# Performance work log

Hardware: AMD Instinct MI355X
Metric: run time of the kernel (lower is better)

Reference implementation:

```python
import jax, jax.numpy as jnp
import numpy as np

B, S, E, H = 4, 2048, 512, 8
DK = E // H  # 64 quantum wires per head


def setup_inputs() -> dict:
    key = jax.random.key(0)
    k1, k2, k3, k4 = jax.random.split(key, 4)
    x = jax.random.normal(k1, (B, S, E), dtype=jnp.float32)
    theta = jax.random.normal(k2, (DK,), dtype=jnp.float32)
    W = jax.random.normal(k3, (E, E), dtype=jnp.float32) * (1.0 / np.sqrt(E))
    b = jax.random.normal(k4, (E,), dtype=jnp.float32) * 0.01
    return {"x": x, "theta": theta, "W": W, "b": b}


def _quantum_project(x, theta):
    # x: [B,S,E] -> heads [B,H,S,DK]. Circuit per wire: RX(x_i) then RX(theta_i),
    # product state => <Z_i> = cos(x_i + theta_i).
    xh = x.reshape(B, S, H, DK).transpose(0, 2, 1, 3)  # [B,H,S,DK]
    return jnp.cos(xh + theta)


def reference(x, theta, W, b):
    q = _quantum_project(x, theta)
    k = _quantum_project(x, theta)
    v = _quantum_project(x, theta)
    scores = jnp.einsum('bhqd,bhkd->bhqk', q, k) / jnp.sqrt(jnp.float32(DK))
    attn = jax.nn.softmax(scores, axis=-1)  # dropout is identity in eval
    out = jnp.einsum('bhqk,bhkd->bhqd', attn, v)  # [B,H,S,DK]
    out = out.transpose(0, 2, 1, 3).reshape(B, S, E)
    return out @ W.T + b
```

## Files before the change

kernel.cpp:

```cpp
#include <hip/hip_runtime.h>
#include <hip/hip_bf16.h>
#include <math.h>

#define B_ 4
#define S_ 2048
#define E_ 512
#define H_ 8
#define DK_ 64

typedef __attribute__((ext_vector_type(8))) short short8;
typedef __attribute__((ext_vector_type(4))) float f32x4;
typedef _Float16 half8 __attribute__((ext_vector_type(8)));
typedef _Float16 half4 __attribute__((ext_vector_type(4)));

__device__ inline short8 ld8(const void* p) {
  return *reinterpret_cast<const short8*>(p);
}

static __device__ inline short8 cvt8h(float4 a, float4 b) {
  half8 r;
  r[0] = (_Float16)a.x; r[1] = (_Float16)a.y; r[2] = (_Float16)a.z; r[3] = (_Float16)a.w;
  r[4] = (_Float16)b.x; r[5] = (_Float16)b.y; r[6] = (_Float16)b.z; r[7] = (_Float16)b.w;
  return __builtin_bit_cast(short8, r);
}

__global__ __launch_bounds__(256) void prep_g_kernel(
    const float* __restrict__ x, const float* __restrict__ theta,
    _Float16* __restrict__ g, _Float16* __restrict__ gTh) {
  int bh = blockIdx.y;
  int b = bh >> 3, h = bh & 7;
  int s0 = blockIdx.x * 64;
  __shared__ _Float16 tile[64][68];
  int tid = threadIdx.x;
  const float* xp = x + ((size_t)(b * S_ + s0)) * E_ + h * DK_;
  _Float16* gp = g + ((size_t)bh * S_ + s0) * DK_;
#pragma unroll
  for (int it = 0; it < 16; ++it) {
    int idx = it * 256 + tid;
    int sr = idx >> 6, dc = idx & 63;
    float val = __cosf(xp[(size_t)sr * E_ + dc] + theta[dc]);
    gp[sr * DK_ + dc] = (_Float16)val;
    tile[sr][dc] = (_Float16)val;
  }
  __syncthreads();
  _Float16* gTp = gTh + ((size_t)bh * DK_) * S_ + s0;
#pragma unroll
  for (int it = 0; it < 16; ++it) {
    int idx = it * 256 + tid;
    int dr = idx >> 6, sc = idx & 63;
    gTp[(size_t)dr * S_ + sc] = tile[sc][dr];
  }
}

__global__ __launch_bounds__(256, 3) void attn_kernel(
    const _Float16* __restrict__ g, const _Float16* __restrict__ gTh,
    _Float16* __restrict__ ao) {
  const int tid = threadIdx.x;
  const int wave = tid >> 6, lane = tid & 63;
  const int col = lane & 15, quad = lane >> 4;
  const int bh = blockIdx.y;
  const int q0 = blockIdx.x * 64;
  const _Float16* gp = g + (size_t)bh * S_ * DK_;
  const _Float16* gvp = gTh + (size_t)bh * DK_ * S_;

  __shared__ short smem[2 * 64 * 72];
  short* kt = smem;
  short* vt = smem + 64 * 72;

  const int srow = tid >> 3;
  const int soct = (tid & 7) * 8;
  const int sd0 = srow * 72 + soct;
  const int sd1 = (srow + 32) * 72 + soct;
  const _Float16* kg0 = gp + tid * 8;
  const _Float16* kg1 = gp + (tid + 256) * 8;
  const _Float16* vg0 = gvp + (size_t)srow * S_ + (tid & 7) * 8;
  const _Float16* vg1 = gvp + (size_t)(srow + 32) * S_ + (tid & 7) * 8;

  short8 kr0 = ld8(kg0), kr1 = ld8(kg1), vr0 = ld8(vg0), vr1 = ld8(vg1);

  *reinterpret_cast<short8*>(kt + sd0) = ld8(gp + (size_t)q0 * DK_ + tid * 8);
  *reinterpret_cast<short8*>(kt + sd1) = ld8(gp + (size_t)q0 * DK_ + (tid + 256) * 8);
  __syncthreads();
  const _Float16 hC1 = (_Float16)0.18033688011112042f;
  half8 qa[4][2];
#pragma unroll
  for (int qc = 0; qc < 4; ++qc) {
    const short* qp = kt + (qc * 16 + col) * 72 + quad * 8;
    qa[qc][0] = *reinterpret_cast<const half8*>(qp) * hC1;
    qa[qc][1] = *reinterpret_cast<const half8*>(qp + 32) * hC1;
  }
  __syncthreads();

  f32x4 o[4][4];
#pragma unroll
  for (int qc = 0; qc < 4; ++qc)
#pragma unroll
    for (int dc = 0; dc < 4; ++dc) o[qc][dc] = f32x4{0.f, 0.f, 0.f, 0.f};
  float l[4] = {0.f, 0.f, 0.f, 0.f};

  for (int kk = 0; kk < S_; kk += 64) {
    *reinterpret_cast<short8*>(kt + sd0) = kr0;
    *reinterpret_cast<short8*>(kt + sd1) = kr1;
    *reinterpret_cast<short8*>(vt + sd0) = vr0;
    *reinterpret_cast<short8*>(vt + sd1) = vr1;
    __syncthreads();

    if (kk + 64 < S_) {
      kr0 = ld8(kg0 + (kk + 64) * 64);
      kr1 = ld8(kg1 + (kk + 64) * 64);
      vr0 = ld8(vg0 + kk + 64);
      vr1 = ld8(vg1 + kk + 64);
    }

    const short* kp = kt + (wave * 16 + col) * 72 + quad * 8;
    half8 kf0 = *reinterpret_cast<const half8*>(kp);
    half8 kf1 = *reinterpret_cast<const half8*>(kp + 32);

    half4 pf[4];
#pragma unroll
    for (int qc = 0; qc < 4; ++qc) {
      f32x4 z{0.f, 0.f, 0.f, 0.f};
      z = __builtin_amdgcn_mfma_f32_16x16x32_f16(kf0, qa[qc][0], z, 0, 0, 0);
      z = __builtin_amdgcn_mfma_f32_16x16x32_f16(kf1, qa[qc][1], z, 0, 0, 0);
      float p0 = __builtin_amdgcn_exp2f(z[0]);
      float p1 = __builtin_amdgcn_exp2f(z[1]);
      float p2 = __builtin_amdgcn_exp2f(z[2]);
      float p3 = __builtin_amdgcn_exp2f(z[3]);
      l[qc] += (p0 + p1) + (p2 + p3);
      half4 pk;
      pk[0] = (_Float16)p0; pk[1] = (_Float16)p1;
      pk[2] = (_Float16)p2; pk[3] = (_Float16)p3;
      pf[qc] = pk;
    }

#pragma unroll
    for (int dc = 0; dc < 4; ++dc) {
      half4 vf = *reinterpret_cast<const half4*>(
          vt + (dc * 16 + col) * 72 + wave * 16 + quad * 4);
#pragma unroll
      for (int qc = 0; qc < 4; ++qc)
        o[qc][dc] = __builtin_amdgcn_mfma_f32_16x16x16f16(vf, pf[qc], o[qc][dc], 0, 0, 0);
    }
    __syncthreads();
  }

#pragma unroll
  for (int qc = 0; qc < 4; ++qc) {
    float t = l[qc];
    t += __shfl_xor(t, 16);
    t += __shfl_xor(t, 32);
    l[qc] = t;
  }
  float* red = (float*)smem;
  if (quad == 0) {
#pragma unroll
    for (int qc = 0; qc < 4; ++qc) red[(wave * 4 + qc) * 16 + col] = l[qc];
  }
  __syncthreads();
  float ltot = 0.f;
#pragma unroll
  for (int w2 = 0; w2 < 4; ++w2) ltot += red[(w2 * 4 + wave) * 16 + col];
  float inv = __builtin_amdgcn_rcpf(ltot);

  int b = bh >> 3, h = bh & 7;
  float* ored = (float*)smem;
#pragma unroll
  for (int qc = 0; qc < 4; ++qc) {
    __syncthreads();
#pragma unroll
    for (int dc = 0; dc < 4; ++dc)
      *reinterpret_cast<f32x4*>(ored + wave * 1024 + lane * 16 + dc * 4) = o[qc][dc];
    __syncthreads();
    if (wave == qc) {
      _Float16* op = ao + ((size_t)b * S_ + (q0 + qc * 16 + col)) * E_ + h * DK_;
#pragma unroll
      for (int dc = 0; dc < 4; ++dc) {
        f32x4 acc = *reinterpret_cast<const f32x4*>(ored + lane * 16 + dc * 4);
#pragma unroll
        for (int w2 = 1; w2 < 4; ++w2)
          acc = acc + *reinterpret_cast<const f32x4*>(ored + w2 * 1024 + lane * 16 + dc * 4);
        half4 pk;
        pk[0] = (_Float16)(acc[0] * inv);
        pk[1] = (_Float16)(acc[1] * inv);
        pk[2] = (_Float16)(acc[2] * inv);
        pk[3] = (_Float16)(acc[3] * inv);
        *reinterpret_cast<half4*>(op + dc * 16 + quad * 4) = pk;
      }
    }
  }
}

__global__ __launch_bounds__(256) void proj_kernel(
    const _Float16* __restrict__ ao, const float* __restrict__ W,
    const float* __restrict__ bias, float* __restrict__ out) {
  const int tid = threadIdx.x;
  const int wave = tid >> 6, lane = tid & 63;
  const int col = lane & 15, quad = lane >> 4;
  const int m0 = blockIdx.x * 64;
  const int n0 = blockIdx.y * 64;
  __shared__ short at[64 * 136];
  __shared__ short bt[64 * 136];

  const int srw = tid >> 4;
  const int soff = (tid & 15) * 8;

  short8 ap_[4];
  float4 wp_[4][2];
#pragma unroll
  for (int it = 0; it < 4; ++it) {
    int row = it * 16 + srw;
    ap_[it] = ld8(ao + (size_t)(m0 + row) * E_ + soff);
    wp_[it][0] = *reinterpret_cast<const float4*>(W + (size_t)(n0 + row) * E_ + soff);
    wp_[it][1] = *reinterpret_cast<const float4*>(W + (size_t)(n0 + row) * E_ + soff + 4);
  }

  f32x4 acc[4] = {{0.f,0.f,0.f,0.f},{0.f,0.f,0.f,0.f},{0.f,0.f,0.f,0.f},{0.f,0.f,0.f,0.f}};

  for (int k0 = 0; k0 < E_; k0 += 128) {
#pragma unroll
    for (int it = 0; it < 4; ++it) {
      int row = it * 16 + srw;
      *reinterpret_cast<short8*>(at + row * 136 + soff) = ap_[it];
      *reinterpret_cast<short8*>(bt + row * 136 + soff) = cvt8h(wp_[it][0], wp_[it][1]);
    }
    __syncthreads();
    if (k0 + 128 < E_) {
#pragma unroll
      for (int it = 0; it < 4; ++it) {
        int row = it * 16 + srw;
        ap_[it] = ld8(ao + (size_t)(m0 + row) * E_ + k0 + 128 + soff);
        wp_[it][0] = *reinterpret_cast<const float4*>(W + (size_t)(n0 + row) * E_ + k0 + 128 + soff);
        wp_[it][1] = *reinterpret_cast<const float4*>(W + (size_t)(n0 + row) * E_ + k0 + 132 + soff);
      }
    }
#pragma unroll
    for (int ks = 0; ks < 4; ++ks) {
      const short* ap = at + (wave * 16 + col) * 136 + ks * 32 + quad * 8;
      half8 a = *reinterpret_cast<const half8*>(ap);
#pragma unroll
      for (int f = 0; f < 4; ++f) {
        const short* bp = bt + (f * 16 + col) * 136 + ks * 32 + quad * 8;
        half8 bb = *reinterpret_cast<const half8*>(bp);
        acc[f] = __builtin_amdgcn_mfma_f32_16x16x32_f16(a, bb, acc[f], 0, 0, 0);
      }
    }
    __syncthreads();
  }

#pragma unroll
  for (int f = 0; f < 4; ++f) {
    float bv = bias[n0 + f * 16 + col];
#pragma unroll
    for (int r = 0; r < 4; ++r) {
      int row = m0 + wave * 16 + quad * 4 + r;
      out[(size_t)row * E_ + n0 + f * 16 + col] = acc[f][r] + bv;
    }
  }
}

extern "C" void kernel_launch(void* const* d_in, const int* in_sizes, int n_in,
                              void* d_out, int out_size, void* d_ws, size_t ws_size,
                              hipStream_t stream) {
  const float* x = (const float*)d_in[0];
  const float* theta = (const float*)d_in[1];
  const float* W = (const float*)d_in[2];
  const float* bias = (const float*)d_in[3];
  float* out = (float*)d_out;
  char* ws = (char*)d_ws;
  const size_t gsz = (size_t)B_ * H_ * S_ * DK_ * 2;
  _Float16* g = (_Float16*)ws;
  _Float16* gTh = (_Float16*)(ws + gsz);
  _Float16* ao = (_Float16*)(ws + 2 * gsz);

  prep_g_kernel<<<dim3(S_ / 64, B_ * H_), 256, 0, stream>>>(x, theta, g, gTh);
  attn_kernel<<<dim3(S_ / 64, B_ * H_), 256, 0, stream>>>(g, gTh, ao);
  proj_kernel<<<dim3((B_ * S_) / 64, E_ / 64), 256, 0, stream>>>(ao, W, bias, out);
}
```

Baseline: 137.1 us.

## Pre-swizzle K/V into MFMA fragment layout and drop LDS staging in attention

The prep kernel now writes K and V into a fragment-native blocked layout, so each wave loads its MFMA operands straight from global memory with no LDS tiles and no per-iteration barriers. The attention loop switches to 32-key blocks per wave using the 16x16x32 MFMA for both QK and PV, and packs P with cvt_pkrtz. W is also converted to fp16 once in a separate kernel, so the projection streams half-width weights instead of converting in the inner loop. The tradeoffs are an extra kernel launch, reliance on L2/global bandwidth for K/V in place of shared-memory reuse, and a changed mapping of query rows onto lanes in the output path.

```diff
diff --git a/kernel.cpp b/kernel.cpp
--- a/kernel.cpp
+++ b/kernel.cpp
@@ -12,84 +12,103 @@
 typedef __attribute__((ext_vector_type(4))) float f32x4;
 typedef _Float16 half8 __attribute__((ext_vector_type(8)));
 typedef _Float16 half4 __attribute__((ext_vector_type(4)));
+typedef __fp16 fp16x2 __attribute__((ext_vector_type(2)));
+typedef unsigned uint4v __attribute__((ext_vector_type(4)));
 
 __device__ inline short8 ld8(const void* p) {
   return *reinterpret_cast<const short8*>(p);
 }
-
-static __device__ inline short8 cvt8h(float4 a, float4 b) {
-  half8 r;
-  r[0] = (_Float16)a.x; r[1] = (_Float16)a.y; r[2] = (_Float16)a.z; r[3] = (_Float16)a.w;
-  r[4] = (_Float16)b.x; r[5] = (_Float16)b.y; r[6] = (_Float16)b.z; r[7] = (_Float16)b.w;
-  return __builtin_bit_cast(short8, r);
-}
+__device__ inline half8 ld8h(const void* p) {
+  return *reinterpret_cast<const half8*>(p);
+}
+
+static __device__ inline unsigned pk2(float a, float b) {
+  fp16x2 h = __builtin_amdgcn_cvt_pkrtz(a, b);
+  return __builtin_bit_cast(unsigned, h);
+}
+static __device__ inline half8 pack8(float p0, float p1, float p2, float p3,
+                                     float p4, float p5, float p6, float p7) {
+  uint4v u;
+  u[0] = pk2(p0, p1); u[1] = pk2(p2, p3);
+  u[2] = pk2(p4, p5); u[3] = pk2(p6, p7);
+  return __builtin_bit_cast(half8, u);
+}
+
 
 __global__ __launch_bounds__(256) void prep_g_kernel(
     const float* __restrict__ x, const float* __restrict__ theta,
-    _Float16* __restrict__ g, _Float16* __restrict__ gTh) {
-  int bh = blockIdx.y;
-  int b = bh >> 3, h = bh & 7;
-  int s0 = blockIdx.x * 64;
-  __shared__ _Float16 tile[64][68];
-  int tid = threadIdx.x;
+    _Float16* __restrict__ kA, _Float16* __restrict__ vA) {
+  const int bh = blockIdx.y;
+  const int b = bh >> 3, h = bh & 7;
+  const int s0 = blockIdx.x * 64;
+  const int tid = threadIdx.x;
+  const int wave = tid >> 6, lane = tid & 63;
+  const int col = lane & 15, quad = lane >> 4;
+  __shared__ _Float16 tile[64 * 72];
+
   const float* xp = x + ((size_t)(b * S_ + s0)) * E_ + h * DK_;
-  _Float16* gp = g + ((size_t)bh * S_ + s0) * DK_;
 #pragma unroll
   for (int it = 0; it < 16; ++it) {
     int idx = it * 256 + tid;
     int sr = idx >> 6, dc = idx & 63;
-    float val = __cosf(xp[(size_t)sr * E_ + dc] + theta[dc]);
-    gp[sr * DK_ + dc] = (_Float16)val;
-    tile[sr][dc] = (_Float16)val;
+    tile[sr * 72 + dc] = (_Float16)__cosf(xp[(size_t)sr * E_ + dc] + theta[dc]);
   }
   __syncthreads();
-  _Float16* gTp = gTh + ((size_t)bh * DK_) * S_ + s0;
-#pragma unroll
-  for (int it = 0; it < 16; ++it) {
-    int idx = it * 256 + tid;
-    int dr = idx >> 6, sc = idx & 63;
-    gTp[(size_t)dr * S_ + sc] = tile[sc][dr];
-  }
+
+  _Float16* kb = kA + (size_t)bh * (S_ * DK_);
+  _Float16* vb = vA + (size_t)bh * (S_ * DK_);
+  const int Gbase = s0 >> 5;
+#pragma unroll
+  for (int it2 = 0; it2 < 2; ++it2) {
+    int c = wave + it2 * 4;
+    int Gl = c >> 2, g = (c >> 1) & 1, hh = c & 1;
+    int ploc = Gl * 32 + ((col >> 2) << 3) + g * 4 + (col & 3);
+    half8 v = ld8h(tile + ploc * 72 + hh * 32 + quad * 8);
+    *reinterpret_cast<half8*>(
+        kb + ((size_t)(Gbase + Gl) * 2048 + (g * 2 + hh) * 512 + lane * 8)) = v;
+  }
+#pragma unroll
+  for (int it2 = 0; it2 < 2; ++it2) {
+    int c = wave + it2 * 4;
+    int Gl = c >> 2, dcc = c & 3;
+    half8 v;
+#pragma unroll
+    for (int j = 0; j < 8; ++j)
+      v[j] = tile[(Gl * 32 + quad * 8 + j) * 72 + dcc * 16 + col];
+    *reinterpret_cast<half8*>(
+        vb + ((size_t)(Gbase + Gl) * 2048 + dcc * 512 + lane * 8)) = v;
+  }
+}
+
+__global__ void prep_w_kernel(const float* __restrict__ W, _Float16* __restrict__ wb) {
+  int i = (blockIdx.x * 256 + threadIdx.x) * 8;
+  float4 a = *reinterpret_cast<const float4*>(W + i);
+  float4 c = *reinterpret_cast<const float4*>(W + i + 4);
+  half8 v;
+  v[0]=(_Float16)a.x; v[1]=(_Float16)a.y; v[2]=(_Float16)a.z; v[3]=(_Float16)a.w;
+  v[4]=(_Float16)c.x; v[5]=(_Float16)c.y; v[6]=(_Float16)c.z; v[7]=(_Float16)c.w;
+  *reinterpret_cast<half8*>(wb + i) = v;
 }
 
 __global__ __launch_bounds__(256, 3) void attn_kernel(
-    const _Float16* __restrict__ g, const _Float16* __restrict__ gTh,
+    const _Float16* __restrict__ kA, const _Float16* __restrict__ vA,
     _Float16* __restrict__ ao) {
   const int tid = threadIdx.x;
   const int wave = tid >> 6, lane = tid & 63;
   const int col = lane & 15, quad = lane >> 4;
   const int bh = blockIdx.y;
   const int q0 = blockIdx.x * 64;
-  const _Float16* gp = g + (size_t)bh * S_ * DK_;
-  const _Float16* gvp = gTh + (size_t)bh * DK_ * S_;
-
-  __shared__ short smem[2 * 64 * 72];
-  short* kt = smem;
-  short* vt = smem + 64 * 72;
-
-  const int srow = tid >> 3;
-  const int soct = (tid & 7) * 8;
-  const int sd0 = srow * 72 + soct;
-  const int sd1 = (srow + 32) * 72 + soct;
-  const _Float16* kg0 = gp + tid * 8;
-  const _Float16* kg1 = gp + (tid + 256) * 8;
-  const _Float16* vg0 = gvp + (size_t)srow * S_ + (tid & 7) * 8;
-  const _Float16* vg1 = gvp + (size_t)(srow + 32) * S_ + (tid & 7) * 8;
-
-  short8 kr0 = ld8(kg0), kr1 = ld8(kg1), vr0 = ld8(vg0), vr1 = ld8(vg1);
-
-  *reinterpret_cast<short8*>(kt + sd0) = ld8(gp + (size_t)q0 * DK_ + tid * 8);
-  *reinterpret_cast<short8*>(kt + sd1) = ld8(gp + (size_t)q0 * DK_ + (tid + 256) * 8);
-  __syncthreads();
+  const _Float16* kb = kA + (size_t)bh * (S_ * DK_);
+  const _Float16* vb = vA + (size_t)bh * (S_ * DK_);
+
   const _Float16 hC1 = (_Float16)0.18033688011112042f;
   half8 qa[4][2];
 #pragma unroll
-  for (int qc = 0; qc < 4; ++qc) {
-    const short* qp = kt + (qc * 16 + col) * 72 + quad * 8;
-    qa[qc][0] = *reinterpret_cast<const half8*>(qp) * hC1;
-    qa[qc][1] = *reinterpret_cast<const half8*>(qp + 32) * hC1;
-  }
-  __syncthreads();
+  for (int qc = 0; qc < 4; ++qc)
+#pragma unroll
+    for (int hh = 0; hh < 2; ++hh)
+      qa[qc][hh] = ld8h(kb + (size_t)((q0 >> 5) + (qc >> 1)) * 2048 +
+                        ((qc & 1) * 2 + hh) * 512 + lane * 8) * hC1;
 
   f32x4 o[4][4];
 #pragma unroll
@@ -98,52 +117,50 @@
     for (int dc = 0; dc < 4; ++dc) o[qc][dc] = f32x4{0.f, 0.f, 0.f, 0.f};
   float l[4] = {0.f, 0.f, 0.f, 0.f};
 
-  for (int kk = 0; kk < S_; kk += 64) {
-    *reinterpret_cast<short8*>(kt + sd0) = kr0;
-    *reinterpret_cast<short8*>(kt + sd1) = kr1;
-    *reinterpret_cast<short8*>(vt + sd0) = vr0;
-    *reinterpret_cast<short8*>(vt + sd1) = vr1;
-    __syncthreads();
-
-    if (kk + 64 < S_) {
-      kr0 = ld8(kg0 + (kk + 64) * 64);
-      kr1 = ld8(kg1 + (kk + 64) * 64);
-      vr0 = ld8(vg0 + kk + 64);
-      vr1 = ld8(vg1 + kk + 64);
-    }
-
-    const short* kp = kt + (wave * 16 + col) * 72 + quad * 8;
-    half8 kf0 = *reinterpret_cast<const half8*>(kp);
-    half8 kf1 = *reinterpret_cast<const half8*>(kp + 32);
-
-    half4 pf[4];
+  const _Float16* kw = kb + (size_t)wave * 16 * 2048 + lane * 8;
+  const _Float16* vw = vb + (size_t)wave * 16 * 2048 + lane * 8;
+
+  for (int it = 0; it < 16; ++it) {
+    const _Float16* kit = kw + it * 2048;
+    const _Float16* vit = vw + it * 2048;
+    half8 kf00 = ld8h(kit);
+    half8 kf01 = ld8h(kit + 512);
+    half8 kf10 = ld8h(kit + 1024);
+    half8 kf11 = ld8h(kit + 1536);
+    half8 vf0 = ld8h(vit);
+    half8 vf1 = ld8h(vit + 512);
+    half8 vf2 = ld8h(vit + 1024);
+    half8 vf3 = ld8h(vit + 1536);
+
+    half8 pf[4];
 #pragma unroll
     for (int qc = 0; qc < 4; ++qc) {
-      f32x4 z{0.f, 0.f, 0.f, 0.f};
-      z = __builtin_amdgcn_mfma_f32_16x16x32_f16(kf0, qa[qc][0], z, 0, 0, 0);
-      z = __builtin_amdgcn_mfma_f32_16x16x32_f16(kf1, qa[qc][1], z, 0, 0, 0);
-      float p0 = __builtin_amdgcn_exp2f(z[0]);
-      float p1 = __builtin_amdgcn_exp2f(z[1]);
-      float p2 = __builtin_amdgcn_exp2f(z[2]);
-      float p3 = __builtin_amdgcn_exp2f(z[3]);
-      l[qc] += (p0 + p1) + (p2 + p3);
-      half4 pk;
-      pk[0] = (_Float16)p0; pk[1] = (_Float16)p1;
-      pk[2] = (_Float16)p2; pk[3] = (_Float16)p3;
-      pf[qc] = pk;
-    }
-
-#pragma unroll
-    for (int dc = 0; dc < 4; ++dc) {
-      half4 vf = *reinterpret_cast<const half4*>(
-          vt + (dc * 16 + col) * 72 + wave * 16 + quad * 4);
-#pragma unroll
-      for (int qc = 0; qc < 4; ++qc)
-        o[qc][dc] = __builtin_amdgcn_mfma_f32_16x16x16f16(vf, pf[qc], o[qc][dc], 0, 0, 0);
-    }
-    __syncthreads();
-  }
-
+      f32x4 z0{0.f, 0.f, 0.f, 0.f}, z1{0.f, 0.f, 0.f, 0.f};
+      z0 = __builtin_amdgcn_mfma_f32_16x16x32_f16(kf00, qa[qc][0], z0, 0, 0, 0);
+      z0 = __builtin_amdgcn_mfma_f32_16x16x32_f16(kf01, qa[qc][1], z0, 0, 0, 0);
+      z1 = __builtin_amdgcn_mfma_f32_16x16x32_f16(kf10, qa[qc][0], z1, 0, 0, 0);
+      z1 = __builtin_amdgcn_mfma_f32_16x16x32_f16(kf11, qa[qc][1], z1, 0, 0, 0);
+      float p0 = __builtin_amdgcn_exp2f(z0[0]);
+      float p1 = __builtin_amdgcn_exp2f(z0[1]);
+      float p2 = __builtin_amdgcn_exp2f(z0[2]);
+      float p3 = __builtin_amdgcn_exp2f(z0[3]);
+      float p4 = __builtin_amdgcn_exp2f(z1[0]);
+      float p5 = __builtin_amdgcn_exp2f(z1[1]);
+      float p6 = __builtin_amdgcn_exp2f(z1[2]);
+      float p7 = __builtin_amdgcn_exp2f(z1[3]);
+      l[qc] += ((p0 + p1) + (p2 + p3)) + ((p4 + p5) + (p6 + p7));
+      pf[qc] = pack8(p0, p1, p2, p3, p4, p5, p6, p7);
+    }
+#pragma unroll
+    for (int qc = 0; qc < 4; ++qc) {
+      o[qc][0] = __builtin_amdgcn_mfma_f32_16x16x32_f16(vf0, pf[qc], o[qc][0], 0, 0, 0);
+      o[qc][1] = __builtin_amdgcn_mfma_f32_16x16x32_f16(vf1, pf[qc], o[qc][1], 0, 0, 0);
+      o[qc][2] = __builtin_amdgcn_mfma_f32_16x16x32_f16(vf2, pf[qc], o[qc][2], 0, 0, 0);
+      o[qc][3] = __builtin_amdgcn_mfma_f32_16x16x32_f16(vf3, pf[qc], o[qc][3], 0, 0, 0);
+    }
+  }
+
+  __shared__ float reds[4096];
 #pragma unroll
   for (int qc = 0; qc < 4; ++qc) {
     float t = l[qc];
@@ -151,47 +168,46 @@
     t += __shfl_xor(t, 32);
     l[qc] = t;
   }
-  float* red = (float*)smem;
   if (quad == 0) {
 #pragma unroll
-    for (int qc = 0; qc < 4; ++qc) red[(wave * 4 + qc) * 16 + col] = l[qc];
+    for (int qc = 0; qc < 4; ++qc) reds[(wave * 4 + qc) * 16 + col] = l[qc];
   }
   __syncthreads();
   float ltot = 0.f;
 #pragma unroll
-  for (int w2 = 0; w2 < 4; ++w2) ltot += red[(w2 * 4 + wave) * 16 + col];
+  for (int w2 = 0; w2 < 4; ++w2) ltot += reds[(w2 * 4 + wave) * 16 + col];
   float inv = __builtin_amdgcn_rcpf(ltot);
 
-  int b = bh >> 3, h = bh & 7;
-  float* ored = (float*)smem;
+  const int b = bh >> 3, h = bh & 7;
+  const int qrow = q0 + ((wave >> 1) << 5) + ((col >> 2) << 3) + (wave & 1) * 4 + (col & 3);
+  _Float16* op = ao + ((size_t)b * S_ + qrow) * E_ + h * DK_;
 #pragma unroll
   for (int qc = 0; qc < 4; ++qc) {
     __syncthreads();
 #pragma unroll
     for (int dc = 0; dc < 4; ++dc)
-      *reinterpret_cast<f32x4*>(ored + wave * 1024 + lane * 16 + dc * 4) = o[qc][dc];
+      *reinterpret_cast<f32x4*>(reds + wave * 1024 + lane * 16 + dc * 4) = o[qc][dc];
     __syncthreads();
     if (wave == qc) {
-      _Float16* op = ao + ((size_t)b * S_ + (q0 + qc * 16 + col)) * E_ + h * DK_;
 #pragma unroll
       for (int dc = 0; dc < 4; ++dc) {
-        f32x4 acc = *reinterpret_cast<const f32x4*>(ored + lane * 16 + dc * 4);
+        f32x4 acc = *reinterpret_cast<const f32x4*>(reds + lane * 16 + dc * 4);
 #pragma unroll
         for (int w2 = 1; w2 < 4; ++w2)
-          acc = acc + *reinterpret_cast<const f32x4*>(ored + w2 * 1024 + lane * 16 + dc * 4);
-        half4 pk;
-        pk[0] = (_Float16)(acc[0] * inv);
-        pk[1] = (_Float16)(acc[1] * inv);
-        pk[2] = (_Float16)(acc[2] * inv);
-        pk[3] = (_Float16)(acc[3] * inv);
-        *reinterpret_cast<half4*>(op + dc * 16 + quad * 4) = pk;
+          acc = acc + *reinterpret_cast<const f32x4*>(reds + w2 * 1024 + lane * 16 + dc * 4);
+        half4 pk4;
+        pk4[0] = (_Float16)(acc[0] * inv);
+        pk4[1] = (_Float16)(acc[1] * inv);
+        pk4[2] = (_Float16)(acc[2] * inv);
+        pk4[3] = (_Float16)(acc[3] * inv);
+        *reinterpret_cast<half4*>(op + dc * 16 + quad * 4) = pk4;
       }
     }
   }
 }
 
 __global__ __launch_bounds__(256) void proj_kernel(
-    const _Float16* __restrict__ ao, const float* __restrict__ W,
+    const _Float16* __restrict__ ao, const _Float16* __restrict__ wb,
     const float* __restrict__ bias, float* __restrict__ out) {
   const int tid = threadIdx.x;
   const int wave = tid >> 6, lane = tid & 63;
@@ -204,14 +220,12 @@
   const int srw = tid >> 4;
   const int soff = (tid & 15) * 8;
 
-  short8 ap_[4];
-  float4 wp_[4][2];
+  short8 ap_[4], wp_[4];
 #pragma unroll
   for (int it = 0; it < 4; ++it) {
     int row = it * 16 + srw;
     ap_[it] = ld8(ao + (size_t)(m0 + row) * E_ + soff);
-    wp_[it][0] = *reinterpret_cast<const float4*>(W + (size_t)(n0 + row) * E_ + soff);
-    wp_[it][1] = *reinterpret_cast<const float4*>(W + (size_t)(n0 + row) * E_ + soff + 4);
+    wp_[it] = ld8(wb + (size_t)(n0 + row) * E_ + soff);
   }
 
   f32x4 acc[4] = {{0.f,0.f,0.f,0.f},{0.f,0.f,0.f,0.f},{0.f,0.f,0.f,0.f},{0.f,0.f,0.f,0.f}};
@@ -221,7 +235,7 @@
     for (int it = 0; it < 4; ++it) {
       int row = it * 16 + srw;
       *reinterpret_cast<short8*>(at + row * 136 + soff) = ap_[it];
-      *reinterpret_cast<short8*>(bt + row * 136 + soff) = cvt8h(wp_[it][0], wp_[it][1]);
+      *reinterpret_cast<short8*>(bt + row * 136 + soff) = wp_[it];
     }
     __syncthreads();
     if (k0 + 128 < E_) {
@@ -229,18 +243,15 @@
       for (int it = 0; it < 4; ++it) {
         int row = it * 16 + srw;
         ap_[it] = ld8(ao + (size_t)(m0 + row) * E_ + k0 + 128 + soff);
-        wp_[it][0] = *reinterpret_cast<const float4*>(W + (size_t)(n0 + row) * E_ + k0 + 128 + soff);
-        wp_[it][1] = *reinterpret_cast<const float4*>(W + (size_t)(n0 + row) * E_ + k0 + 132 + soff);
+        wp_[it] = ld8(wb + (size_t)(n0 + row) * E_ + k0 + 128 + soff);
       }
     }
 #pragma unroll
     for (int ks = 0; ks < 4; ++ks) {
-      const short* ap = at + (wave * 16 + col) * 136 + ks * 32 + quad * 8;
-      half8 a = *reinterpret_cast<const half8*>(ap);
+      half8 a = *reinterpret_cast<const half8*>(at + (wave * 16 + col) * 136 + ks * 32 + quad * 8);
 #pragma unroll
       for (int f = 0; f < 4; ++f) {
-        const short* bp = bt + (f * 16 + col) * 136 + ks * 32 + quad * 8;
-        half8 bb = *reinterpret_cast<const half8*>(bp);
+        half8 bb = *reinterpret_cast<const half8*>(bt + (f * 16 + col) * 136 + ks * 32 + quad * 8);
         acc[f] = __builtin_amdgcn_mfma_f32_16x16x32_f16(a, bb, acc[f], 0, 0, 0);
       }
     }
@@ -268,11 +279,13 @@
   float* out = (float*)d_out;
   char* ws = (char*)d_ws;
   const size_t gsz = (size_t)B_ * H_ * S_ * DK_ * 2;
-  _Float16* g = (_Float16*)ws;
-  _Float16* gTh = (_Float16*)(ws + gsz);
+  _Float16* kA = (_Float16*)ws;
+  _Float16* vA = (_Float16*)(ws + gsz);
   _Float16* ao = (_Float16*)(ws + 2 * gsz);
-
-  prep_g_kernel<<<dim3(S_ / 64, B_ * H_), 256, 0, stream>>>(x, theta, g, gTh);
-  attn_kernel<<<dim3(S_ / 64, B_ * H_), 256, 0, stream>>>(g, gTh, ao);
-  proj_kernel<<<dim3((B_ * S_) / 64, E_ / 64), 256, 0, stream>>>(ao, W, bias, out);
-}
+  _Float16* wb = (_Float16*)(ws + 3 * gsz);
+
+  prep_g_kernel<<<dim3(S_ / 64, B_ * H_), 256, 0, stream>>>(x, theta, kA, vA);
+  prep_w_kernel<<<dim3((E_ * E_) / (256 * 8)), 256, 0, stream>>>(W, wb);
+  attn_kernel<<<dim3(S_ / 64, B_ * H_), 256, 0, stream>>>(kA, vA, ao);
+  proj_kernel<<<dim3((B_ * S_) / 64, E_ / 64), 256, 0, stream>>>(ao, wb, bias, out);
+}
```

New measurement: 129.0 us. -5.9%, faster.
